# Kernel tuning notes

Measured on AMD Instinct MI355X. Metric: run time of the kernel, lower is better.

Reference implementation:

```python
import jax, jax.numpy as jnp
import numpy as np

DIM, NH, T_MAX = 1024, 16, 2048
HD = DIM // NH
EPS = 1e-6


def _rope_tables(T, hd, dtype=jnp.float32):
    inv_freq = 1.0 / (10000.0 ** (jnp.arange(0, hd, 2, dtype=jnp.float32) / hd))
    t = jnp.arange(T, dtype=jnp.float32)
    freqs = jnp.outer(t, inv_freq)                 # [T, hd/2]
    emb = jnp.concatenate([freqs, freqs], axis=-1)  # [T, hd]
    return jnp.cos(emb).astype(dtype), jnp.sin(emb).astype(dtype)


def _rotate_half(x):
    x1, x2 = jnp.split(x, 2, axis=-1)
    return jnp.concatenate([-x2, x1], axis=-1)


def _rmsnorm(x, g):
    rms = jnp.sqrt(jnp.mean(x * x, axis=-1, keepdims=True) + EPS)
    return x / rms * g


def setup_inputs() -> dict:
    key = jax.random.key(0)
    ks = jax.random.split(key, 10)
    B, T, C = 4, 2048, DIM
    s = 1.0 / np.sqrt(C)
    x = jax.random.normal(ks[0], (B, T, C), dtype=jnp.float32)
    mask = jnp.tril(jnp.ones((T, T), dtype=jnp.int32))[None, None, :, :]
    wq = jax.random.normal(ks[1], (C, C), jnp.float32) * s
    wk = jax.random.normal(ks[2], (C, C), jnp.float32) * s
    wv = jax.random.normal(ks[3], (C, C), jnp.float32) * s
    wo = jax.random.normal(ks[4], (C, C), jnp.float32) * s
    w1 = jax.random.normal(ks[5], (C, 4 * C), jnp.float32) * s
    w2 = jax.random.normal(ks[6], (4 * C, C), jnp.float32) * (1.0 / np.sqrt(4 * C))
    w3 = jax.random.normal(ks[7], (C, 4 * C), jnp.float32) * s
    g1 = jnp.ones((C,), jnp.float32)
    g2 = jnp.ones((C,), jnp.float32)
    return {"x": x, "mask": mask, "g1": g1, "wq": wq, "wk": wk, "wv": wv,
            "wo": wo, "g2": g2, "w1": w1, "w2": w2, "w3": w3}


def reference(x, mask, g1, wq, wk, wv, wo, g2, w1, w2, w3):
    B, T, C = x.shape
    scale = HD ** -0.5
    # --- attention sublayer ---
    h = _rmsnorm(x, g1)
    q = (h @ wq).reshape(B, T, NH, HD)
    k = (h @ wk).reshape(B, T, NH, HD)
    v = (h @ wv).reshape(B, T, NH, HD)
    cos, sin = _rope_tables(T, HD, x.dtype)
    cos = cos[None, :, None, :]
    sin = sin[None, :, None, :]
    q = q * cos + _rotate_half(q) * sin
    k = k * cos + _rotate_half(k) * sin
    attn = jnp.einsum("bthd,bshd->bhts", q, k) * scale  # [B,H,T,T]
    attn = jnp.where(mask == 0, -jnp.inf, attn)
    attn = jax.nn.softmax(attn, axis=-1)
    o = jnp.einsum("bhts,bshd->bthd", attn, v).reshape(B, T, C)
    x = x + o @ wo
    # --- SwiGLU FFN sublayer ---
    h = _rmsnorm(x, g2)
    x = x + (jax.nn.silu(h @ w1) * (h @ w3)) @ w2
    return x
```

## Files before the change

### kernel.cpp

```cpp
#include <hip/hip_runtime.h>
#include <cstdint>

typedef unsigned short u16;
typedef __attribute__((ext_vector_type(8))) short bf16x8;
typedef __attribute__((ext_vector_type(4))) float f32x4;

__device__ __forceinline__ u16 f2b(float f) {
  union { float f; unsigned u; } c; c.f = f;
  unsigned u = c.u;
  return (u16)((u + 0x7FFFu + ((u >> 16) & 1u)) >> 16);
}
__device__ __forceinline__ float b2f(u16 b) {
  union { unsigned u; float f; } c; c.u = ((unsigned)b) << 16;
  return c.f;
}

typedef __attribute__((address_space(1))) void gv_t;
typedef __attribute__((address_space(3))) void lv_t;
__device__ __forceinline__ void gload_lds16(const void* g, void* l) {
  __builtin_amdgcn_global_load_lds((gv_t*)g, (lv_t*)l, 16, 0, 0);
}

__global__ void transpose_f2b(const float* __restrict__ in, u16* __restrict__ out,
                              int R, int C) {
  __shared__ float t[32][33];
  const int c0 = blockIdx.x * 32, r0 = blockIdx.y * 32;
  const int tx = threadIdx.x, ty = threadIdx.y;
#pragma unroll
  for (int i = 0; i < 4; ++i)
    t[ty + 8 * i][tx] = in[(size_t)(r0 + ty + 8 * i) * C + c0 + tx];
  __syncthreads();
#pragma unroll
  for (int i = 0; i < 4; ++i)
    out[(size_t)(c0 + ty + 8 * i) * R + r0 + tx] = f2b(t[tx][ty + 8 * i]);
}

__global__ __launch_bounds__(256) void rmsnorm_k(const float* __restrict__ x,
                                                 const float* __restrict__ g,
                                                 u16* __restrict__ out) {
  const int row = blockIdx.x, tid = threadIdx.x;
  const float4 v = ((const float4*)x)[(size_t)row * 256 + tid];
  float ss = v.x * v.x + v.y * v.y + v.z * v.z + v.w * v.w;
#pragma unroll
  for (int off = 1; off < 64; off <<= 1) ss += __shfl_xor(ss, off, 64);
  __shared__ float red[4];
  if ((tid & 63) == 0) red[tid >> 6] = ss;
  __syncthreads();
  const float mean = (red[0] + red[1] + red[2] + red[3]) * (1.0f / 1024.0f);
  const float rinv = 1.0f / sqrtf(mean + 1e-6f);
  const float4 gv = ((const float4*)g)[tid];
  u16* o = out + (size_t)row * 1024 + tid * 4;
  o[0] = f2b(v.x * rinv * gv.x);
  o[1] = f2b(v.y * rinv * gv.y);
  o[2] = f2b(v.z * rinv * gv.z);
  o[3] = f2b(v.w * rinv * gv.w);
}

__global__ __launch_bounds__(256) void rope_k(u16* __restrict__ qkv) {
  const int i = blockIdx.x * 256 + threadIdx.x;
  const int d = i & 31;
  const int h = (i >> 5) & 15;
  const int bt = i >> 9;
  const int t = bt & 2047;
  const float inv = exp2f((float)d * -0.4152410118609203f);
  const float th = (float)t * inv;
  float s, c;
  sincosf(th, &s, &c);
  size_t base = (size_t)bt * 3072 + h * 64 + d;
#pragma unroll
  for (int half = 0; half < 2; ++half) {
    const float x1 = b2f(qkv[base]);
    const float x2 = b2f(qkv[base + 32]);
    qkv[base]      = f2b(x1 * c - x2 * s);
    qkv[base + 32] = f2b(x2 * c + x1 * s);
    base += 1024;
  }
}

__global__ void vtrans_k(const u16* __restrict__ qkv, u16* __restrict__ VT) {
  __shared__ u16 tl[32][34];
  const int t0 = blockIdx.x * 32;
  const int bh = blockIdx.y >> 1;
  const int d0 = (blockIdx.y & 1) * 32;
  const int b = bh >> 4, h = bh & 15;
  const int tx = threadIdx.x, ty = threadIdx.y;
  const u16* src = qkv + (size_t)(b * 2048 + t0) * 3072 + 2048 + h * 64 + d0;
#pragma unroll
  for (int i = 0; i < 4; ++i)
    tl[ty + 8 * i][tx] = src[(size_t)(ty + 8 * i) * 3072 + tx];
  __syncthreads();
  u16* dst = VT + ((size_t)bh * 64 + d0) * 2048 + t0;
#pragma unroll
  for (int i = 0; i < 4; ++i)
    dst[(size_t)(ty + 8 * i) * 2048 + tx] = tl[tx][ty + 8 * i];
}

template <int EPI>
__global__ __launch_bounds__(512, 2)
void gemm256(const u16* __restrict__ A, const u16* __restrict__ BT,
             void* __restrict__ Cout, const float* __restrict__ resid,
             int M, int N, int K, int lda) {
  __shared__ alignas(16) u16 LDS[65536];
  char* const ldsc = (char*)LDS;
  const int tid = threadIdx.x;
  const int wave = tid >> 6, lane = tid & 63;
  const int wr = wave >> 2, wc = wave & 3;
  const int l15 = lane & 15, quad = lane >> 4;
  const int bm = blockIdx.x * 256, bn = blockIdx.y * 256;
  const int NT = K >> 6;

  const int swz = (l15 & 8) << 2;
  const int aoff = (((wr * 64 + l15) * 64 + quad * 16) ^ swz);
  const int boff = (((wc * 32 + l15) * 64 + quad * 16) ^ swz) + 65536;

  const int kperm = ((lane & 3) ^ ((lane >> 5) << 1)) * 8;
  const u16* sA = A + (size_t)(bm + wave * 16 + (lane >> 2)) * lda + kperm;
  const u16* sB = BT + (size_t)(bn + wave * 16 + (lane >> 2)) * K + kperm;
  const size_t hA = (size_t)128 * lda;
  const size_t hB = (size_t)128 * K;
  const int dstW = wave * 1024;

  f32x4 acc[8][4];
#pragma unroll
  for (int m = 0; m < 8; ++m)
#pragma unroll
    for (int n = 0; n < 4; ++n) acc[m][n] = (f32x4){0.f, 0.f, 0.f, 0.f};
  bf16x8 a[4][2], b[4][2];

#define STAGE(kt_, slot_, buf_)                                               \
  if ((kt_) < NT) {                                                           \
    const u16* s_ = (((slot_) & 1) ? sB + ((size_t)((slot_) >> 1)) * hB       \
                                   : sA + ((size_t)((slot_) >> 1)) * hA) +    \
                    (size_t)(kt_) * 64;                                       \
    char* d_ = ldsc + (((slot_) & 1) ? 65536 : 0) + (buf_) * 32768 +          \
               ((slot_) >> 1) * 16384 + dstW;                                 \
    gload_lds16(s_, d_);                                                      \
    gload_lds16(s_ + 32, d_ + 8192);                                          \
  }

#define LOAD_A(mh_, buf_)                                                     \
  _Pragma("unroll") for (int mf = 0; mf < 4; ++mf)                            \
      _Pragma("unroll") for (int kk = 0; kk < 2; ++kk)                        \
          a[mf][kk] = *(const bf16x8*)(ldsc + aoff + (buf_) * 32768 +         \
                                       (mh_) * 16384 + kk * 8192 + mf * 1024);

#define LOAD_B2(buf_)                                                         \
  _Pragma("unroll") for (int nh = 0; nh < 2; ++nh)                            \
      _Pragma("unroll") for (int nf = 0; nf < 2; ++nf)                        \
          _Pragma("unroll") for (int kk = 0; kk < 2; ++kk)                    \
              b[nh * 2 + nf][kk] =                                            \
                  *(const bf16x8*)(ldsc + boff + (buf_) * 32768 +             \
                                   nh * 16384 + kk * 8192 + nf * 1024);

#define MMA2(mh_)                                                             \
  __builtin_amdgcn_s_setprio(1);                                              \
  _Pragma("unroll") for (int mf = 0; mf < 4; ++mf)                            \
      _Pragma("unroll") for (int n = 0; n < 4; ++n)                           \
          _Pragma("unroll") for (int kk = 0; kk < 2; ++kk)                    \
              acc[(mh_) * 4 + mf][n] =                                        \
                  __builtin_amdgcn_mfma_f32_16x16x32_bf16(                    \
                      a[mf][kk], b[n][kk], acc[(mh_) * 4 + mf][n], 0, 0, 0);  \
  __builtin_amdgcn_s_setprio(0);

#define BAR() __builtin_amdgcn_s_barrier()
#define DRAIN_LGKM()                                                          \
  {                                                                           \
    asm volatile("s_waitcnt lgkmcnt(0)" ::: "memory");                        \
    __builtin_amdgcn_sched_barrier(0);                                        \
  }

  STAGE(0, 0, 0); STAGE(0, 1, 0); STAGE(0, 3, 0);
  STAGE(0, 2, 0);
  STAGE(1, 0, 1); STAGE(1, 1, 1); STAGE(1, 3, 1);
  asm volatile("s_waitcnt vmcnt(8)" ::: "memory");
  BAR();

  for (int t = 0; t < NT; ++t) {
    const int bsel = t & 1;
    LOAD_A(0, bsel); LOAD_B2(bsel);
    STAGE(t + 1, 2, bsel ^ 1);
    BAR(); DRAIN_LGKM(); MMA2(0);
    if (t == NT - 1) { asm volatile("s_waitcnt vmcnt(0)" ::: "memory"); }
    else             { asm volatile("s_waitcnt vmcnt(8)" ::: "memory"); }
    BAR();
    LOAD_A(1, bsel);
    STAGE(t + 2, 0, bsel); STAGE(t + 2, 1, bsel); STAGE(t + 2, 3, bsel);
    BAR(); DRAIN_LGKM(); MMA2(1);
    if (t < NT - 2) {
      asm volatile("s_waitcnt vmcnt(8)" ::: "memory");
      BAR();
    } else if (t == NT - 2) {
      asm volatile("s_waitcnt vmcnt(2)" ::: "memory");
      BAR();
    }
  }
#undef STAGE
#undef LOAD_A
#undef LOAD_B2
#undef MMA2

#pragma unroll
  for (int m = 0; m < 8; ++m) {
    const int gr = bm + (m >> 2) * 128 + wr * 64 + (m & 3) * 16 + quad * 4;
#pragma unroll
    for (int n = 0; n < 4; ++n) {
      const int gc = bn + (n >> 1) * 128 + wc * 32 + (n & 1) * 16 + l15;
#pragma unroll
      for (int r = 0; r < 4; ++r) {
        const size_t off = (size_t)(gr + r) * N + gc;
        if (EPI == 0) {
          ((u16*)Cout)[off] = f2b(acc[m][n][r]);
        } else {
          ((float*)Cout)[off] = resid[off] + acc[m][n][r];
        }
      }
    }
  }
#undef BAR
#undef DRAIN_LGKM
}

__global__ __launch_bounds__(512, 2)
void gemm256g(const u16* __restrict__ A, const u16* __restrict__ B1T,
              const u16* __restrict__ B3T, u16* __restrict__ Cout,
              int Ncols, int K, int lda) {
  __shared__ alignas(16) u16 LDS[65536];
  char* const ldsc = (char*)LDS;
  const int tid = threadIdx.x;
  const int wave = tid >> 6, lane = tid & 63;
  const int wr = wave >> 2, wc = wave & 3;
  const int l15 = lane & 15, quad = lane >> 4;
  const int bm = blockIdx.x * 256, bn = blockIdx.y * 128;
  const int NT = K >> 6;

  const int swz = (l15 & 8) << 2;
  const int aoff  = (((wr * 64 + l15) * 64 + quad * 16) ^ swz);
  const int b1off = (((wc * 32 + l15) * 64 + quad * 16) ^ swz) + 65536;

  const int kperm = ((lane & 3) ^ ((lane >> 5) << 1)) * 8;
  const u16* sA  = A   + (size_t)(bm + wave * 16 + (lane >> 2)) * lda + kperm;
  const u16* sB1 = B1T + (size_t)(bn + wave * 16 + (lane >> 2)) * K + kperm;
  const u16* sB3 = B3T + (size_t)(bn + wave * 16 + (lane >> 2)) * K + kperm;
  const size_t hA = (size_t)128 * lda;
  const int dstW = wave * 1024;

  f32x4 acc1[8][2], acc3[8][2];
#pragma unroll
  for (int m = 0; m < 8; ++m)
#pragma unroll
    for (int n = 0; n < 2; ++n) {
      acc1[m][n] = (f32x4){0.f, 0.f, 0.f, 0.f};
      acc3[m][n] = (f32x4){0.f, 0.f, 0.f, 0.f};
    }
  bf16x8 a[4][2], b1[2][2], b3[2][2];

#define STAGE_A(kt_, half_, buf_)                                             \
  if ((kt_) < NT) {                                                           \
    const u16* s_ = sA + (size_t)(half_) * hA + (size_t)(kt_) * 64;           \
    char* d_ = ldsc + (buf_) * 32768 + (half_) * 16384 + dstW;                \
    gload_lds16(s_, d_);                                                      \
    gload_lds16(s_ + 32, d_ + 8192);                                          \
  }
#define STAGE_B1(kt_, buf_)                                                   \
  if ((kt_) < NT) {                                                           \
    const u16* s_ = sB1 + (size_t)(kt_) * 64;                                 \
    char* d_ = ldsc + 65536 + (buf_) * 16384 + dstW;                          \
    gload_lds16(s_, d_);                                                      \
    gload_lds16(s_ + 32, d_ + 8192);                                          \
  }
#define STAGE_B3(kt_, buf_)                                                   \
  if ((kt_) < NT) {                                                           \
    const u16* s_ = sB3 + (size_t)(kt_) * 64;                                 \
    char* d_ = ldsc + 98304 + (buf_) * 16384 + dstW;                          \
    gload_lds16(s_, d_);                                                      \
    gload_lds16(s_ + 32, d_ + 8192);                                          \
  }
#define LOAD_A(mh_, buf_)                                                     \
  _Pragma("unroll") for (int mf = 0; mf < 4; ++mf)                            \
      _Pragma("unroll") for (int kk = 0; kk < 2; ++kk)                        \
          a[mf][kk] = *(const bf16x8*)(ldsc + aoff + (buf_) * 32768 +         \
                                       (mh_) * 16384 + kk * 8192 + mf * 1024);
#define LOAD_B13(buf_)                                                        \
  _Pragma("unroll") for (int nf = 0; nf < 2; ++nf)                            \
      _Pragma("unroll") for (int kk = 0; kk < 2; ++kk) {                      \
        b1[nf][kk] = *(const bf16x8*)(ldsc + b1off + (buf_) * 16384 +         \
                                      kk * 8192 + nf * 1024);                 \
        b3[nf][kk] = *(const bf16x8*)(ldsc + b1off + 32768 +                  \
                                      (buf_) * 16384 + kk * 8192 +            \
                                      nf * 1024);                             \
      }
#define MMAG(mh_)                                                             \
  __builtin_amdgcn_s_setprio(1);                                              \
  _Pragma("unroll") for (int mf = 0; mf < 4; ++mf)                            \
      _Pragma("unroll") for (int nf = 0; nf < 2; ++nf)                        \
          _Pragma("unroll") for (int kk = 0; kk < 2; ++kk) {                  \
            acc1[(mh_) * 4 + mf][nf] =                                        \
                __builtin_amdgcn_mfma_f32_16x16x32_bf16(                      \
                    a[mf][kk], b1[nf][kk], acc1[(mh_) * 4 + mf][nf], 0, 0, 0);\
            acc3[(mh_) * 4 + mf][nf] =                                        \
                __builtin_amdgcn_mfma_f32_16x16x32_bf16(                      \
                    a[mf][kk], b3[nf][kk], acc3[(mh_) * 4 + mf][nf], 0, 0, 0);\
          }                                                                   \
  __builtin_amdgcn_s_setprio(0);
#define BAR() __builtin_amdgcn_s_barrier()
#define DRAIN_LGKM()                                                          \
  {                                                                           \
    asm volatile("s_waitcnt lgkmcnt(0)" ::: "memory");                        \
    __builtin_amdgcn_sched_barrier(0);                                        \
  }

  STAGE_A(0, 0, 0); STAGE_B1(0, 0); STAGE_B3(0, 0);
  STAGE_A(0, 1, 0);
  STAGE_A(1, 0, 1); STAGE_B1(1, 1); STAGE_B3(1, 1);
  asm volatile("s_waitcnt vmcnt(8)" ::: "memory");
  BAR();

  for (int t = 0; t < NT; ++t) {
    const int bsel = t & 1;
    LOAD_A(0, bsel); LOAD_B13(bsel);
    STAGE_A(t + 1, 1, bsel ^ 1);
    BAR(); DRAIN_LGKM(); MMAG(0);
    if (t == NT - 1) { asm volatile("s_waitcnt vmcnt(0)" ::: "memory"); }
    else             { asm volatile("s_waitcnt vmcnt(8)" ::: "memory"); }
    BAR();
    LOAD_A(1, bsel);
    STAGE_A(t + 2, 0, bsel); STAGE_B1(t + 2, bsel); STAGE_B3(t + 2, bsel);
    BAR(); DRAIN_LGKM(); MMAG(1);
    if (t < NT - 2) {
      asm volatile("s_waitcnt vmcnt(8)" ::: "memory");
      BAR();
    } else if (t == NT - 2) {
      asm volatile("s_waitcnt vmcnt(2)" ::: "memory");
      BAR();
    }
  }
#undef STAGE_A
#undef STAGE_B1
#undef STAGE_B3
#undef LOAD_A
#undef LOAD_B13
#undef MMAG
#undef BAR
#undef DRAIN_LGKM

#pragma unroll
  for (int m = 0; m < 8; ++m) {
    const int gr = bm + (m >> 2) * 128 + wr * 64 + (m & 3) * 16 + quad * 4;
#pragma unroll
    for (int n = 0; n < 2; ++n) {
      const int gc = bn + wc * 32 + n * 16 + l15;
#pragma unroll
      for (int r = 0; r < 4; ++r) {
        const float v1 = acc1[m][n][r];
        const float v3 = acc3[m][n][r];
        const float s = v1 / (1.f + __expf(-v1));
        Cout[(size_t)(gr + r) * Ncols + gc] = f2b(s * v3);
      }
    }
  }
}

template <int EPI>
__global__ __launch_bounds__(512, 2)
void gemm256n(const u16* __restrict__ A, const u16* __restrict__ BT,
              void* __restrict__ Cout, const float* __restrict__ resid,
              int M, int N, int K, int lda) {
  __shared__ alignas(16) u16 LDS[49152];
  char* const ldsc = (char*)LDS;
  const int tid = threadIdx.x;
  const int wave = tid >> 6, lane = tid & 63;
  const int wr = wave >> 1, wc = wave & 1;
  const int l15 = lane & 15, quad = lane >> 4;
  const int bm = blockIdx.x * 256, bn = blockIdx.y * 128;
  const int NT = K >> 6;

  const int swz = (l15 & 8) << 2;
  const int aoff = (wr >> 1) * 16384 +
                   ((((wr & 1) * 64 + l15) * 64 + quad * 16) ^ swz);
  const int boff = (((wc * 64 + l15) * 64 + quad * 16) ^ swz) + 65536;

  const int kperm = ((lane & 3) ^ ((lane >> 5) << 1)) * 8;
  const u16* sA = A + (size_t)(bm + wave * 16 + (lane >> 2)) * lda + kperm;
  const u16* sB = BT + (size_t)(bn + wave * 16 + (lane >> 2)) * K + kperm;
  const size_t hA = (size_t)128 * lda;
  const int dstW = wave * 1024;

  f32x4 acc[4][4];
#pragma unroll
  for (int m = 0; m < 4; ++m)
#pragma unroll
    for (int n = 0; n < 4; ++n) acc[m][n] = (f32x4){0.f, 0.f, 0.f, 0.f};
  bf16x8 a[4][2], b[4][2];

#define STAGE_A(kt_, half_, buf_)                                             \
  if ((kt_) < NT) {                                                           \
    const u16* s_ = sA + (size_t)(half_) * hA + (size_t)(kt_) * 64;           \
    char* d_ = ldsc + (buf_) * 32768 + (half_) * 16384 + dstW;                \
    gload_lds16(s_, d_);                                                      \
    gload_lds16(s_ + 32, d_ + 8192);                                          \
  }
#define STAGE_B(kt_, buf_)                                                    \
  if ((kt_) < NT) {                                                           \
    const u16* s_ = sB + (size_t)(kt_) * 64;                                  \
    char* d_ = ldsc + 65536 + (buf_) * 16384 + dstW;                          \
    gload_lds16(s_, d_);                                                      \
    gload_lds16(s_ + 32, d_ + 8192);                                          \
  }
#define LOAD_ALL(buf_)                                                        \
  _Pragma("unroll") for (int mf = 0; mf < 4; ++mf)                            \
      _Pragma("unroll") for (int kk = 0; kk < 2; ++kk)                        \
          a[mf][kk] = *(const bf16x8*)(ldsc + aoff + (buf_) * 32768 +         \
                                       kk * 8192 + mf * 1024);                \
  _Pragma("unroll") for (int nf = 0; nf < 4; ++nf)                            \
      _Pragma("unroll") for (int kk = 0; kk < 2; ++kk)                        \
          b[nf][kk] = *(const bf16x8*)(ldsc + boff + (buf_) * 16384 +         \
                                       kk * 8192 + nf * 1024);
#define MMA_N(nlo_)                                                           \
  __builtin_amdgcn_s_setprio(1);                                              \
  _Pragma("unroll") for (int mf = 0; mf < 4; ++mf)                            \
      _Pragma("unroll") for (int nf = 0; nf < 2; ++nf)                        \
          _Pragma("unroll") for (int kk = 0; kk < 2; ++kk)                    \
              acc[mf][(nlo_) * 2 + nf] =                                      \
                  __builtin_amdgcn_mfma_f32_16x16x32_bf16(                    \
                      a[mf][kk], b[(nlo_) * 2 + nf][kk],                      \
                      acc[mf][(nlo_) * 2 + nf], 0, 0, 0);                     \
  __builtin_amdgcn_s_setprio(0);
#define BAR() __builtin_amdgcn_s_barrier()
#define DRAIN_LGKM()                                                          \
  {                                                                           \
    asm volatile("s_waitcnt lgkmcnt(0)" ::: "memory");                        \
    __builtin_amdgcn_sched_barrier(0);                                        \
  }

  STAGE_A(0, 0, 0); STAGE_A(0, 1, 0); STAGE_B(0, 0);
  STAGE_A(1, 0, 1); STAGE_A(1, 1, 1); STAGE_B(1, 1);
  asm volatile("s_waitcnt vmcnt(6)" ::: "memory");
  BAR();

  for (int t = 0; t < NT; ++t) {
    const int bsel = t & 1;
    LOAD_ALL(bsel);
    BAR(); DRAIN_LGKM();
    MMA_N(0);
    BAR();
    STAGE_A(t + 2, 0, bsel); STAGE_A(t + 2, 1, bsel); STAGE_B(t + 2, bsel);
    MMA_N(1);
    if (t + 2 < NT) {
      asm volatile("s_waitcnt vmcnt(6)" ::: "memory");
      BAR();
    } else if (t + 1 < NT) {
      asm volatile("s_waitcnt vmcnt(0)" ::: "memory");
      BAR();
    }
  }
#undef STAGE_A
#undef STAGE_B
#undef LOAD_ALL
#undef MMA_N
#undef BAR
#undef DRAIN_LGKM

#pragma unroll
  for (int m = 0; m < 4; ++m) {
    const int gr = bm + wr * 64 + m * 16 + quad * 4;
#pragma unroll
    for (int n = 0; n < 4; ++n) {
      const int gc = bn + wc * 64 + n * 16 + l15;
#pragma unroll
      for (int r = 0; r < 4; ++r) {
        const size_t off = (size_t)(gr + r) * N + gc;
        if (EPI == 0) {
          ((u16*)Cout)[off] = f2b(acc[m][n][r]);
        } else {
          ((float*)Cout)[off] = resid[off] + acc[m][n][r];
        }
      }
    }
  }
}

__global__ __launch_bounds__(256)
void attn_kernel(const u16* __restrict__ QKV, const u16* __restrict__ VT,
                 u16* __restrict__ O, float* __restrict__ Opart,
                 float* __restrict__ Spart) {
  const int T = 2048, stQ = 3072;
  const int tid = threadIdx.x, wave = tid >> 6, lane = tid & 63;
  const int l15 = lane & 15, quad = lane >> 4;

  const int xi = (int)blockIdx.x;
  const bool split = (xi < 22);
  const int qt = split ? (15 - (xi >> 1)) : (26 - xi);
  const int chunk = split ? (xi & 1) : 0;
  const int len = split ? (qt + 1) : (2 * qt + 2);
  const int kt0 = chunk * (qt + 1);
  const int ktEnd = kt0 + len;

  const int qb0 = qt * 128;
  const int bh = blockIdx.y, b = bh >> 4, h = bh & 15;
  const float sc2 = 0.125f * 1.44269504088896f;
  const float M0 = 32.0f;

  __shared__ alignas(16) u16 Kf[2][8 * 512];
  __shared__ alignas(16) u16 Vf[2][8 * 512];
  __shared__ alignas(16) u16 Pl[4][2][16 * 72];

  const u16* Qb  = QKV + (size_t)b * T * stQ + h * 64;
  const u16* Kb  = Qb + 1024;
  const u16* VTb = VT + (size_t)bh * 64 * T;

  const int r0 = qb0 + wave * 16;
  const int r1 = r0 + 64;
  const u16* qp0 = Qb + (size_t)(r0 + l15) * stQ + quad * 8;
  const u16* qp1 = Qb + (size_t)(r1 + l15) * stQ + quad * 8;
  const bf16x8 qf00 = *(const bf16x8*)qp0;
  const bf16x8 qf01 = *(const bf16x8*)(qp0 + 32);
  const bf16x8 qf10 = *(const bf16x8*)qp1;
  const bf16x8 qf11 = *(const bf16x8*)(qp1 + 32);

  bf16x8 ones;
#pragma unroll
  for (int j = 0; j < 8; ++j) ones[j] = (short)0x3F80;

  const u16* kS = Kb + (size_t)(wave * 16 + l15) * stQ + quad * 8;
  const u16* vS = VTb + (size_t)(wave * 16 + l15) * T + quad * 8;

  f32x4 o0[4], o1[4], sum0, sum1;
#pragma unroll
  for (int c = 0; c < 4; ++c) {
    o0[c] = (f32x4){0.f, 0.f, 0.f, 0.f};
    o1[c] = (f32x4){0.f, 0.f, 0.f, 0.f};
  }
  sum0 = (f32x4){0.f, 0.f, 0.f, 0.f};
  sum1 = (f32x4){0.f, 0.f, 0.f, 0.f};

  u16* pw0 = &Pl[wave][0][0];
  u16* pw1 = &Pl[wave][1][0];

  gload_lds16(kS + (size_t)(kt0 * 64) * stQ,      &Kf[0][(wave * 2 + 0) * 512]);
  gload_lds16(kS + (size_t)(kt0 * 64) * stQ + 32, &Kf[0][(wave * 2 + 1) * 512]);
  gload_lds16(vS + (size_t)(kt0 * 64),            &Vf[0][(wave * 2 + 0) * 512]);
  gload_lds16(vS + (size_t)(kt0 * 64) + 32,       &Vf[0][(wave * 2 + 1) * 512]);

  for (int kt = kt0; kt < ktEnd; ++kt) {
    const int kb0 = kt * 64;
    const int buf = (kt - kt0) & 1;
    __builtin_amdgcn_sched_barrier(0);
    if (kt + 1 < ktEnd) {
      const size_t kb1 = (size_t)(kb0 + 64);
      gload_lds16(kS + kb1 * stQ,      &Kf[buf ^ 1][(wave * 2 + 0) * 512]);
      gload_lds16(kS + kb1 * stQ + 32, &Kf[buf ^ 1][(wave * 2 + 1) * 512]);
      gload_lds16(vS + kb1,            &Vf[buf ^ 1][(wave * 2 + 0) * 512]);
      gload_lds16(vS + kb1 + 32,       &Vf[buf ^ 1][(wave * 2 + 1) * 512]);
      asm volatile("s_waitcnt vmcnt(4)" ::: "memory");
    } else {
      asm volatile("s_waitcnt vmcnt(0)" ::: "memory");
    }
    __builtin_amdgcn_s_barrier();
    __builtin_amdgcn_sched_barrier(0);

    bf16x8 kf[8], vf[8];
#pragma unroll
    for (int g = 0; g < 8; ++g) {
      kf[g] = *(const bf16x8*)(&Kf[buf][g * 512 + lane * 8]);
      vf[g] = *(const bf16x8*)(&Vf[buf][g * 512 + lane * 8]);
    }

    const bool act0 = (kb0 <= r0 + 15);

    {
      f32x4 s[4];
      __builtin_amdgcn_s_setprio(1);
#pragma unroll
      for (int jj = 0; jj < 4; ++jj) {
        s[jj] = (f32x4){0.f, 0.f, 0.f, 0.f};
        s[jj] = __builtin_amdgcn_mfma_f32_16x16x32_bf16(qf10, kf[jj * 2 + 0], s[jj], 0, 0, 0);
        s[jj] = __builtin_amdgcn_mfma_f32_16x16x32_bf16(qf11, kf[jj * 2 + 1], s[jj], 0, 0, 0);
      }
      __builtin_amdgcn_s_setprio(0);
      if (kb0 + 63 > r1) {
#pragma unroll
        for (int jj = 0; jj < 4; ++jj)
#pragma unroll
          for (int r = 0; r < 4; ++r) {
            const bool msk = (kb0 + jj * 16 + l15) > (r1 + quad * 4 + r);
            const float a = msk ? -1e30f : (s[jj][r] * sc2 - M0);
            pw1[(quad * 4 + r) * 72 + jj * 16 + l15] = f2b(exp2f(a));
          }
      } else {
#pragma unroll
        for (int jj = 0; jj < 4; ++jj)
#pragma unroll
          for (int r = 0; r < 4; ++r)
            pw1[(quad * 4 + r) * 72 + jj * 16 + l15] =
                f2b(exp2f(s[jj][r] * sc2 - M0));
      }
    }
    if (act0) {
      f32x4 s[4];
      __builtin_amdgcn_s_setprio(1);
#pragma unroll
      for (int jj = 0; jj < 4; ++jj) {
        s[jj] = (f32x4){0.f, 0.f, 0.f, 0.f};
        s[jj] = __builtin_amdgcn_mfma_f32_16x16x32_bf16(qf00, kf[jj * 2 + 0], s[jj], 0, 0, 0);
        s[jj] = __builtin_amdgcn_mfma_f32_16x16x32_bf16(qf01, kf[jj * 2 + 1], s[jj], 0, 0, 0);
      }
      __builtin_amdgcn_s_setprio(0);
      if (kb0 + 63 > r0) {
#pragma unroll
        for (int jj = 0; jj < 4; ++jj)
#pragma unroll
          for (int r = 0; r < 4; ++r) {
            const bool msk = (kb0 + jj * 16 + l15) > (r0 + quad * 4 + r);
            const float a = msk ? -1e30f : (s[jj][r] * sc2 - M0);
            pw0[(quad * 4 + r) * 72 + jj * 16 + l15] = f2b(exp2f(a));
          }
      } else {
#pragma unroll
        for (int jj = 0; jj < 4; ++jj)
#pragma unroll
          for (int r = 0; r < 4; ++r)
            pw0[(quad * 4 + r) * 72 + jj * 16 + l15] =
                f2b(exp2f(s[jj][r] * sc2 - M0));
      }
    }

    const bf16x8 pf10 = *(const bf16x8*)(pw1 + l15 * 72 + quad * 8);
    const bf16x8 pf11 = *(const bf16x8*)(pw1 + l15 * 72 + 32 + quad * 8);
    __builtin_amdgcn_s_setprio(1);
#pragma unroll
    for (int c = 0; c < 4; ++c) {
      o1[c] = __builtin_amdgcn_mfma_f32_16x16x32_bf16(pf10, vf[c * 2 + 0], o1[c], 0, 0, 0);
      o1[c] = __builtin_amdgcn_mfma_f32_16x16x32_bf16(pf11, vf[c * 2 + 1], o1[c], 0, 0, 0);
    }
    sum1 = __builtin_amdgcn_mfma_f32_16x16x32_bf16(pf10, ones, sum1, 0, 0, 0);
    sum1 = __builtin_amdgcn_mfma_f32_16x16x32_bf16(pf11, ones, sum1, 0, 0, 0);
    __builtin_amdgcn_s_setprio(0);
    if (act0) {
      const bf16x8 pf00 = *(const bf16x8*)(pw0 + l15 * 72 + quad * 8);
      const bf16x8 pf01 = *(const bf16x8*)(pw0 + l15 * 72 + 32 + quad * 8);
      __builtin_amdgcn_s_setprio(1);
#pragma unroll
      for (int c = 0; c < 4; ++c) {
        o0[c] = __builtin_amdgcn_mfma_f32_16x16x32_bf16(pf00, vf[c * 2 + 0], o0[c], 0, 0, 0);
        o0[c] = __builtin_amdgcn_mfma_f32_16x16x32_bf16(pf01, vf[c * 2 + 1], o0[c], 0, 0, 0);
      }
      sum0 = __builtin_amdgcn_mfma_f32_16x16x32_bf16(pf00, ones, sum0, 0, 0, 0);
      sum0 = __builtin_amdgcn_mfma_f32_16x16x32_bf16(pf01, ones, sum0, 0, 0, 0);
      __builtin_amdgcn_s_setprio(0);
    }
    __builtin_amdgcn_s_barrier();
  }

  if (split) {
    const int pi = (bh * 11 + (qt - 5)) * 2 + chunk;
    float* Po = Opart + (size_t)pi * 8192;
    float* Ps = Spart + (size_t)pi * 128;
    const int lr0 = wave * 16 + quad * 4;
#pragma unroll
    for (int c = 0; c < 4; ++c)
#pragma unroll
      for (int r = 0; r < 4; ++r) {
        Po[(lr0 + r) * 64 + c * 16 + l15]      = o0[c][r];
        Po[(64 + lr0 + r) * 64 + c * 16 + l15] = o1[c][r];
      }
    if (l15 == 0) {
#pragma unroll
      for (int r = 0; r < 4; ++r) {
        Ps[lr0 + r]      = sum0[r];
        Ps[64 + lr0 + r] = sum1[r];
      }
    }
  } else {
    float i0[4], i1[4];
#pragma unroll
    for (int r = 0; r < 4; ++r) { i0[r] = 1.f / sum0[r]; i1[r] = 1.f / sum1[r]; }
    u16* op0 = O + ((size_t)(b * T) + r0 + quad * 4) * 1024 + h * 64 + l15;
    u16* op1 = O + ((size_t)(b * T) + r1 + quad * 4) * 1024 + h * 64 + l15;
#pragma unroll
    for (int c = 0; c < 4; ++c)
#pragma unroll
      for (int r = 0; r < 4; ++r) {
        op0[(size_t)r * 1024 + c * 16] = f2b(o0[c][r] * i0[r]);
        op1[(size_t)r * 1024 + c * 16] = f2b(o1[c][r] * i1[r]);
      }
  }
}

__global__ __launch_bounds__(256)
void attn_combine(const float* __restrict__ Opart, const float* __restrict__ Spart,
                  u16* __restrict__ O) {
  const int sp = blockIdx.x;
  const int bh = sp / 11, qt = 5 + (sp % 11);
  const int b = bh >> 4, h = bh & 15;
  const int t = threadIdx.x;
  const int row = t >> 1, ch = (t & 1) * 32;
  const size_t p0 = (size_t)(2 * sp) * 8192, p1 = p0 + 8192;
  const float s = Spart[(size_t)(2 * sp) * 128 + row] +
                  Spart[(size_t)(2 * sp) * 128 + 128 + row];
  const float inv = 1.f / s;
  const float4* A  = (const float4*)(Opart + p0 + row * 64 + ch);
  const float4* Bv = (const float4*)(Opart + p1 + row * 64 + ch);
  u16* op = O + ((size_t)(b * 2048) + qt * 128 + row) * 1024 + h * 64 + ch;
#pragma unroll
  for (int j = 0; j < 8; ++j) {
    const float4 a = A[j], bb = Bv[j];
    op[j * 4 + 0] = f2b((a.x + bb.x) * inv);
    op[j * 4 + 1] = f2b((a.y + bb.y) * inv);
    op[j * 4 + 2] = f2b((a.z + bb.z) * inv);
    op[j * 4 + 3] = f2b((a.w + bb.w) * inv);
  }
}

extern "C" void kernel_launch(void* const* d_in, const int* in_sizes, int n_in,
                              void* d_out, int out_size, void* d_ws, size_t ws_size,
                              hipStream_t stream) {
  const float* x  = (const float*)d_in[0];
  const float* g1 = (const float*)d_in[2];
  const float* wq = (const float*)d_in[3];
  const float* wk = (const float*)d_in[4];
  const float* wv = (const float*)d_in[5];
  const float* wo = (const float*)d_in[6];
  const float* g2 = (const float*)d_in[7];
  const float* w1 = (const float*)d_in[8];
  const float* w2 = (const float*)d_in[9];
  const float* w3 = (const float*)d_in[10];
  float* out = (float*)d_out;

  const int T = 2048, NH = 16, B = 4;
  const int M = B * T;
  const size_t MB = 1ull << 20;

  char* ws = (char*)d_ws;
  u16* hb    = (u16*)(ws);
  u16* wqkvT = (u16*)(ws + 16 * MB);
  u16* woT   = (u16*)(ws + 22 * MB);
  u16* w13T  = (u16*)(ws + 24 * MB);
  u16* w2T   = (u16*)(ws + 40 * MB);
  u16* qkv   = (u16*)(ws + 48 * MB);
  u16* VT    = (u16*)(ws + 96 * MB);
  u16* Ob    = (u16*)(ws + 112 * MB);
  u16* a13g  = (u16*)(ws + 48 * MB);
  float* Opart = (float*)(ws + 128 * MB);
  float* Spart = Opart + (size_t)1408 * 8192;

  const dim3 tb(32, 8);
  transpose_f2b<<<dim3(32, 32),  tb, 0, stream>>>(wq, wqkvT,              1024, 1024);
  transpose_f2b<<<dim3(32, 32),  tb, 0, stream>>>(wk, wqkvT + 1024*1024,  1024, 1024);
  transpose_f2b<<<dim3(32, 32),  tb, 0, stream>>>(wv, wqkvT + 2048*1024,  1024, 1024);
  transpose_f2b<<<dim3(32, 32),  tb, 0, stream>>>(wo, woT, 1024, 1024);
  transpose_f2b<<<dim3(128, 32), tb, 0, stream>>>(w1, w13T,               1024, 4096);
  transpose_f2b<<<dim3(128, 32), tb, 0, stream>>>(w3, w13T + 4096*1024,   1024, 4096);
  transpose_f2b<<<dim3(32, 128), tb, 0, stream>>>(w2, w2T, 4096, 1024);

  rmsnorm_k<<<M, 256, 0, stream>>>(x, g1, hb);

  gemm256<0><<<dim3(32, 12), 512, 0, stream>>>(hb, wqkvT, qkv, nullptr, M, 3072, 1024, 1024);

  rope_k<<<16384, 256, 0, stream>>>(qkv);
  vtrans_k<<<dim3(64, 128), tb, 0, stream>>>(qkv, VT);

  attn_kernel<<<dim3(27, B * NH), 256, 0, stream>>>(qkv, VT, Ob, Opart, Spart);
  attn_combine<<<dim3(704), 256, 0, stream>>>(Opart, Spart, Ob);

  gemm256n<1><<<dim3(32, 8), 512, 0, stream>>>(Ob, woT, out, x, M, 1024, 1024, 1024);

  rmsnorm_k<<<M, 256, 0, stream>>>(out, g2, hb);

  gemm256g<<<dim3(32, 32), 512, 0, stream>>>(hb, w13T, w13T + (size_t)4096 * 1024,
                                             a13g, 4096, 1024, 1024);

  gemm256n<1><<<dim3(32, 8), 512, 0, stream>>>(a13g, w2T, out, out, M, 1024, 4096, 4096);
}
```

Baseline: 637.9 us.

## Rebalance causal attention work with table-driven split-K across up to three chunks

Replaces the two-way split of long query tiles with a precomputed schedule of 36 work items per head. Each item covers a contiguous range of at most about 11 key tiles, and short tiles are packed together, so per-block work is more uniform and the tail of the launch is shorter. The combine kernel now sums two or three partial results per tile. Partial buffers are split across two workspace regions, one of them reusing the hb region, which costs more partial-buffer traffic and a slightly longer combine step.

Result: slower. 705.5 us (+10.6%).

```diff
diff --git a/kernel.cpp b/kernel.cpp
--- a/kernel.cpp
+++ b/kernel.cpp
@@ -20,6 +20,19 @@
 __device__ __forceinline__ void gload_lds16(const void* g, void* l) {
   __builtin_amdgcn_global_load_lds((gv_t*)g, (lv_t*)l, 16, 0, 0);
 }
+
+__device__ const int ATT_QT[36]  = {15,15,15,14,14,14,13,13,13,12,12,12,
+                                    11,11,11,10, 7, 7, 3,10,10, 9, 9, 6,
+                                     6, 9, 8, 8, 8, 5, 5, 2, 4, 4, 1, 0};
+__device__ const int ATT_KT0[36] = { 0,11,22, 0,10,20, 0,10,19, 0, 9,18,
+                                     0, 8,16, 0, 0, 8, 0, 8,15, 0, 7, 0,
+                                     7,14, 0, 6,12, 0, 6, 0, 0, 5, 0, 0};
+__device__ const int ATT_LEN[36] = {11,11,10,10,10,10,10, 9, 9, 9, 9, 8,
+                                     8, 8, 8, 8, 8, 8, 8, 7, 7, 7, 7, 7,
+                                     7, 6, 6, 6, 6, 6, 6, 6, 5, 5, 4, 2};
+__device__ const int ATT_PIX[36] = { 0, 1, 2, 3, 4, 5, 6, 7, 8, 9,10,11,
+                                    12,13,14,15,24,25,-1,16,17,18,19,26,
+                                    27,20,21,22,23,28,29,-1,30,31,-1,-1};
 
 __global__ void transpose_f2b(const float* __restrict__ in, u16* __restrict__ out,
                               int R, int C) {
@@ -481,22 +494,22 @@
 
 __global__ __launch_bounds__(256)
 void attn_kernel(const u16* __restrict__ QKV, const u16* __restrict__ VT,
-                 u16* __restrict__ O, float* __restrict__ Opart,
-                 float* __restrict__ Spart) {
+                 u16* __restrict__ O, float* __restrict__ OpA,
+                 float* __restrict__ SpA, float* __restrict__ OpB,
+                 float* __restrict__ SpB) {
   const int T = 2048, stQ = 3072;
   const int tid = threadIdx.x, wave = tid >> 6, lane = tid & 63;
   const int l15 = lane & 15, quad = lane >> 4;
 
   const int xi = (int)blockIdx.x;
-  const bool split = (xi < 22);
-  const int qt = split ? (15 - (xi >> 1)) : (26 - xi);
-  const int chunk = split ? (xi & 1) : 0;
-  const int len = split ? (qt + 1) : (2 * qt + 2);
-  const int kt0 = chunk * (qt + 1);
-  const int ktEnd = kt0 + len;
+  const int bh = (int)blockIdx.y;
+  const int qt = ATT_QT[xi];
+  const int kt0 = ATT_KT0[xi];
+  const int ktEnd = kt0 + ATT_LEN[xi];
+  const int pidx = ATT_PIX[xi];
 
   const int qb0 = qt * 128;
-  const int bh = blockIdx.y, b = bh >> 4, h = bh & 15;
+  const int b = bh >> 4, h = bh & 15;
   const float sc2 = 0.125f * 1.44269504088896f;
   const float M0 = 32.0f;
 
@@ -651,10 +664,12 @@
     __builtin_amdgcn_s_barrier();
   }
 
-  if (split) {
-    const int pi = (bh * 11 + (qt - 5)) * 2 + chunk;
-    float* Po = Opart + (size_t)pi * 8192;
-    float* Ps = Spart + (size_t)pi * 128;
+  if (pidx >= 0) {
+    const int g = bh * 32 + pidx;
+    float* Po = (g < 1400) ? OpA + (size_t)g * 8192
+                           : OpB + (size_t)(g - 1400) * 8192;
+    float* Ps = (g < 1400) ? SpA + (size_t)g * 128
+                           : SpB + (size_t)(g - 1400) * 128;
     const int lr0 = wave * 16 + quad * 4;
 #pragma unroll
     for (int c = 0; c < 4; ++c)
@@ -687,27 +702,41 @@
 }
 
 __global__ __launch_bounds__(256)
-void attn_combine(const float* __restrict__ Opart, const float* __restrict__ Spart,
+void attn_combine(const float* __restrict__ OpA, const float* __restrict__ SpA,
+                  const float* __restrict__ OpB, const float* __restrict__ SpB,
                   u16* __restrict__ O) {
   const int sp = blockIdx.x;
-  const int bh = sp / 11, qt = 5 + (sp % 11);
+  const int bh = sp / 12, j = sp % 12;
+  const int qt = 15 - j;
+  const int pb = (j < 8) ? 3 * j : 24 + 2 * (j - 8);
+  const int nch = (j < 8) ? 3 : 2;
   const int b = bh >> 4, h = bh & 15;
   const int t = threadIdx.x;
   const int row = t >> 1, ch = (t & 1) * 32;
-  const size_t p0 = (size_t)(2 * sp) * 8192, p1 = p0 + 8192;
-  const float s = Spart[(size_t)(2 * sp) * 128 + row] +
-                  Spart[(size_t)(2 * sp) * 128 + 128 + row];
-  const float inv = 1.f / s;
-  const float4* A  = (const float4*)(Opart + p0 + row * 64 + ch);
-  const float4* Bv = (const float4*)(Opart + p1 + row * 64 + ch);
+
+  float S = 0.f;
+  for (int c = 0; c < nch; ++c) {
+    const int g = bh * 32 + pb + c;
+    const float* Sv = (g < 1400) ? SpA + (size_t)g * 128
+                                 : SpB + (size_t)(g - 1400) * 128;
+    S += Sv[row];
+  }
+  const float inv = 1.f / S;
   u16* op = O + ((size_t)(b * 2048) + qt * 128 + row) * 1024 + h * 64 + ch;
 #pragma unroll
-  for (int j = 0; j < 8; ++j) {
-    const float4 a = A[j], bb = Bv[j];
-    op[j * 4 + 0] = f2b((a.x + bb.x) * inv);
-    op[j * 4 + 1] = f2b((a.y + bb.y) * inv);
-    op[j * 4 + 2] = f2b((a.z + bb.z) * inv);
-    op[j * 4 + 3] = f2b((a.w + bb.w) * inv);
+  for (int jj = 0; jj < 8; ++jj) {
+    float ax = 0.f, ay = 0.f, az = 0.f, aw = 0.f;
+    for (int c = 0; c < nch; ++c) {
+      const int g = bh * 32 + pb + c;
+      const float* Ov = (g < 1400) ? OpA + (size_t)g * 8192
+                                   : OpB + (size_t)(g - 1400) * 8192;
+      const float4 a = ((const float4*)(Ov + row * 64 + ch))[jj];
+      ax += a.x; ay += a.y; az += a.z; aw += a.w;
+    }
+    op[jj * 4 + 0] = f2b(ax * inv);
+    op[jj * 4 + 1] = f2b(ay * inv);
+    op[jj * 4 + 2] = f2b(az * inv);
+    op[jj * 4 + 3] = f2b(aw * inv);
   }
 }
 
@@ -740,8 +769,10 @@
   u16* VT    = (u16*)(ws + 96 * MB);
   u16* Ob    = (u16*)(ws + 112 * MB);
   u16* a13g  = (u16*)(ws + 48 * MB);
-  float* Opart = (float*)(ws + 128 * MB);
-  float* Spart = Opart + (size_t)1408 * 8192;
+  float* OpA = (float*)(ws + 128 * MB);
+  float* SpA = OpA + (size_t)1400 * 8192;
+  float* OpB = (float*)(ws);
+  float* SpB = OpB + (size_t)648 * 8192;
 
   const dim3 tb(32, 8);
   transpose_f2b<<<dim3(32, 32),  tb, 0, stream>>>(wq, wqkvT,              1024, 1024);
@@ -759,8 +790,8 @@
   rope_k<<<16384, 256, 0, stream>>>(qkv);
   vtrans_k<<<dim3(64, 128), tb, 0, stream>>>(qkv, VT);
 
-  attn_kernel<<<dim3(27, B * NH), 256, 0, stream>>>(qkv, VT, Ob, Opart, Spart);
-  attn_combine<<<dim3(704), 256, 0, stream>>>(Opart, Spart, Ob);
+  attn_kernel<<<dim3(36, B * NH), 256, 0, stream>>>(qkv, VT, Ob, OpA, SpA, OpB, SpB);
+  attn_combine<<<dim3(768), 256, 0, stream>>>(OpA, SpA, OpB, SpB, Ob);
 
   gemm256n<1><<<dim3(32, 8), 512, 0, stream>>>(Ob, woT, out, x, M, 1024, 1024, 1024);
 
```
